# Optimization experiments

Measured on AMD Instinct MI355X. Metric: run time of the kernel, lower is better.

Reference implementation:

```python
import math
import jax, jax.numpy as jnp
import numpy as np

B, NQ, NKV, D, H = 32, 512, 512, 1024, 8
DH = D // H              # 128
N_COLS = 512             # n + 1
D_COL = math.ceil(2 * math.log2(N_COLS))  # 18


def setup_inputs() -> dict:
    key = jax.random.key(0)
    ks = jax.random.split(key, 8)
    s = 0.02
    return {
        "x_q": jax.random.normal(ks[0], (B, NQ, D), jnp.float32),
        "x_kv": jax.random.normal(ks[1], (B, NKV, D), jnp.float32),
        # sym_weight=True => W_tail is W_head (shared)
        "W_head_w": jax.random.normal(ks[2], (D, D), jnp.float32) * s,
        "W_head_b": jnp.zeros((D,), jnp.float32),
        "W_v_w": jax.random.normal(ks[3], (D, D), jnp.float32) * s,
        "W_v_b": jnp.zeros((D,), jnp.float32),
        "W_out_w": jax.random.normal(ks[4], (D, D), jnp.float32) * s,
        "W_out_b": jnp.zeros((D,), jnp.float32),
        "rel_emb": jnp.ones((H, DH), jnp.float32),
        "col_head": jax.random.normal(ks[5], (H, N_COLS, D_COL), jnp.float32) * 0.2,
        "col_tail": jax.random.normal(ks[6], (H, N_COLS, D_COL), jnp.float32) * 0.2,
    }


def _heads(x, W, b, h, dh):
    # Linear then split heads: [B, n, d] -> [B, H, n, dh]
    B_, n, _ = x.shape
    y = x @ W.T + b
    return y.reshape(B_, n, h, dh).transpose(0, 2, 1, 3)


def reference(x_q, x_kv, W_head_w, W_head_b, W_v_w, W_v_b,
              W_out_w, W_out_b, rel_emb, col_head, col_tail):
    Bb, nq, d = x_q.shape
    nkv = x_kv.shape[1]
    h, dh = rel_emb.shape

    f_head = _heads(x_q, W_head_w, W_head_b, h, dh) * rel_emb[None, :, None, :]
    f_tail = _heads(x_kv, W_head_w, W_head_b, h, dh) * rel_emb[None, :, None, :]  # W_tail = W_head (sym_weight)
    f_v = _heads(x_kv, W_v_w, W_v_b, h, dh)

    # content score: [B, H, nq, nkv]
    weight_score = jnp.einsum('bhqd,bhkd->bhqk', f_head, f_tail) / math.sqrt(dh)

    # learned column topology: [H, n_cols, n_cols]
    adj_logits = jnp.einsum('hqc,hkc->hqk', col_head, col_tail)
    eye = jnp.eye(adj_logits.shape[-1], dtype=bool)  # nsi: zero diagonal before softmax
    adj_logits = jnp.where(eye[None], 0.0, adj_logits)
    adj = jax.nn.softmax(adj_logits, axis=-1)[:, :nq, :nkv]

    adj_mask = (1.0 - adj) * -10000.0
    fr_graph = jax.nn.softmax(weight_score + adj_mask[None], axis=-1)

    x = jnp.einsum('bhqk,bhkd->bhqd', fr_graph, f_v)
    x = x.transpose(0, 2, 1, 3).reshape(Bb, nq, h * dh)
    x = x @ W_out_w.T + W_out_b
    return (x, fr_graph.reshape(Bb * h, nq, nkv))
```

## Files before the change

### kernel.cpp

```cpp
#include <hip/hip_runtime.h>

typedef __attribute__((ext_vector_type(8))) __bf16 bf8;
typedef __attribute__((ext_vector_type(4))) __bf16 bf4;
typedef __attribute__((ext_vector_type(4))) float f32x4;

#define DEVI static __device__ __forceinline__

DEVI void gload_lds16(const void* g, void* l) {
  __builtin_amdgcn_global_load_lds(
      (const __attribute__((address_space(1))) unsigned int*)g,
      (__attribute__((address_space(3))) unsigned int*)l, 16, 0, 0);
}

__global__ __launch_bounds__(256) void cvt_kernel(const float* __restrict__ in,
                                                  __bf16* __restrict__ out, int n4) {
  int stride = gridDim.x * blockDim.x;
  for (int i = blockIdx.x * blockDim.x + threadIdx.x; i < n4; i += stride) {
    f32x4 v = reinterpret_cast<const f32x4*>(in)[i];
    bf4 o;
    o[0] = (__bf16)v[0]; o[1] = (__bf16)v[1]; o[2] = (__bf16)v[2]; o[3] = (__bf16)v[3];
    reinterpret_cast<bf4*>(out)[i] = o;
  }
}

template <int MODE>
__global__ __launch_bounds__(256) void gemm_proj(
    const __bf16* __restrict__ A, const __bf16* __restrict__ Bw,
    const float* __restrict__ bias, const float* __restrict__ rel,
    __bf16* __restrict__ obf, float* __restrict__ of32) {
  __shared__ alignas(16) __bf16 As[128 * 64];
  __shared__ alignas(16) __bf16 Bs[128 * 64];
  const int tid = threadIdx.x;
  const int lane = tid & 63;
  const int wave = tid >> 6;
  const int wr = wave >> 1, wc = wave & 1;
  const int lr = lane & 15, lk = (lane >> 4) * 8;
  const int bm = blockIdx.x, bn = blockIdx.y;

  f32x4 acc[4][4];
#pragma unroll
  for (int i = 0; i < 4; ++i)
#pragma unroll
    for (int j = 0; j < 4; ++j)
#pragma unroll
      for (int e = 0; e < 4; ++e) acc[i][j][e] = 0.f;

  const __bf16* Ab = A + (size_t)bm * 128 * 1024;
  const __bf16* Bb = Bw + (size_t)bn * 128 * 1024;
  const int sr = tid >> 3;
  const int sc = (tid & 7) * 8;

  for (int kt = 0; kt < 1024; kt += 64) {
#pragma unroll
    for (int i = 0; i < 4; ++i) {
      gload_lds16(Ab + (size_t)(sr + i * 32) * 1024 + kt + sc, As + tid * 8 + i * 2048);
      gload_lds16(Bb + (size_t)(sr + i * 32) * 1024 + kt + sc, Bs + tid * 8 + i * 2048);
    }
    __syncthreads();
#pragma unroll
    for (int kk = 0; kk < 64; kk += 32) {
      bf8 a[4], b[4];
#pragma unroll
      for (int mi = 0; mi < 4; ++mi)
        a[mi] = *reinterpret_cast<const bf8*>(&As[(wr * 64 + mi * 16 + lr) * 64 + kk + lk]);
#pragma unroll
      for (int ni = 0; ni < 4; ++ni)
        b[ni] = *reinterpret_cast<const bf8*>(&Bs[(wc * 64 + ni * 16 + lr) * 64 + kk + lk]);
#pragma unroll
      for (int mi = 0; mi < 4; ++mi)
#pragma unroll
        for (int ni = 0; ni < 4; ++ni)
          acc[mi][ni] = __builtin_amdgcn_mfma_f32_16x16x32_bf16(a[mi], b[ni], acc[mi][ni], 0, 0, 0);
    }
    __syncthreads();
  }

  const int mBase = bm * 128 + wr * 64;
  const int nBase = bn * 128 + wc * 64;
#pragma unroll
  for (int mi = 0; mi < 4; ++mi) {
#pragma unroll
    for (int ni = 0; ni < 4; ++ni) {
      const int n = nBase + ni * 16 + lr;
#pragma unroll
      for (int r = 0; r < 4; ++r) {
        const int m = mBase + mi * 16 + (lane >> 4) * 4 + r;
        float v = acc[mi][ni][r] + bias[n];
        if (MODE == 0) v *= rel[n];
        if (MODE == 2) {
          of32[(size_t)m * 1024 + n] = v;
        } else if (MODE == 0) {
          size_t idx = ((size_t)((m >> 9) * 8 + (n >> 7))) * 65536 +
                       (size_t)(m & 511) * 128 + (n & 127);
          obf[idx] = (__bf16)v;
        } else {
          size_t idx = ((size_t)((m >> 9) * 8 + (n >> 7))) * 65536 +
                       (size_t)(n & 127) * 512 + (m & 511);
          obf[idx] = (__bf16)v;
        }
      }
    }
  }
}

__global__ __launch_bounds__(256) void adj_kernel(const float* __restrict__ ch_all,
                                                  const float* __restrict__ ct_all,
                                                  float* __restrict__ adjT) {
  const int wave = threadIdx.x >> 6, lane = threadIdx.x & 63;
  const int row = blockIdx.x * 4 + wave;
  const int h = row >> 9, i = row & 511;
  float ch[18];
  const float* chp = ch_all + ((size_t)h * 512 + i) * 18;
#pragma unroll
  for (int t = 0; t < 18; ++t) ch[t] = chp[t];
  float e[8];
  float m = -1e30f;
#pragma unroll
  for (int jj = 0; jj < 8; ++jj) {
    const int j = jj * 64 + lane;
    const float* ctp = ct_all + ((size_t)h * 512 + j) * 18;
    float d = 0.f;
#pragma unroll
    for (int t = 0; t < 18; ++t) d += ch[t] * ctp[t];
    if (j == i) d = 0.f;
    e[jj] = d;
    m = fmaxf(m, d);
  }
#pragma unroll
  for (int off = 32; off >= 1; off >>= 1) m = fmaxf(m, __shfl_xor(m, off));
  float s = 0.f;
#pragma unroll
  for (int jj = 0; jj < 8; ++jj) { e[jj] = __expf(e[jj] - m); s += e[jj]; }
#pragma unroll
  for (int off = 32; off >= 1; off >>= 1) s += __shfl_xor(s, off);
  const float inv = 10000.f / s;
  float* op = adjT + (size_t)h * 262144 + i;
#pragma unroll
  for (int jj = 0; jj < 8; ++jj) op[(size_t)(jj * 64 + lane) * 512] = e[jj] * inv;
}

__global__ __launch_bounds__(256, 3) void fused_attn_kernel(
    const __bf16* __restrict__ fh, const __bf16* __restrict__ ft,
    const __bf16* __restrict__ fvT, const float* __restrict__ adjT,
    float* __restrict__ fr, __bf16* __restrict__ ctx) {
  __shared__ alignas(16) __bf16 Bt[128 * 128];
  __shared__ alignas(16) __bf16 Pl[4][16 * 128];
  const int tid = threadIdx.x;
  const int l = tid & 63, w = tid >> 6;
  const int bh = blockIdx.x;
  const int qt = blockIdx.y;
  const int b = bh >> 3, h = bh & 7;
  const int wrow = qt * 64 + w * 16;
  const int lr = l & 15;
  const int khi = l >> 4;

  const int srow = tid >> 4;
  const int scc = (tid & 15) ^ (srow & 7);

  bf8 afr[4];
  {
    const __bf16* ap = fh + (size_t)bh * 65536 + (size_t)(wrow + lr) * 128 + khi * 8;
#pragma unroll
    for (int kk4 = 0; kk4 < 4; ++kk4)
      afr[kk4] = *reinterpret_cast<const bf8*>(ap + kk4 * 32);
  }

  f32x4 acc[32];
#pragma unroll
  for (int n = 0; n < 32; ++n)
#pragma unroll
    for (int e = 0; e < 4; ++e) acc[n][e] = 0.f;

  const __bf16* ftb = ft + (size_t)bh * 65536;
#pragma unroll
  for (int kt = 0; kt < 4; ++kt) {
#pragma unroll
    for (int i = 0; i < 8; ++i)
      gload_lds16(ftb + (size_t)(kt * 128 + i * 16 + srow) * 128 + scc * 8,
                  Bt + i * 2048 + tid * 8);
    __syncthreads();
#pragma unroll
    for (int kk4 = 0; kk4 < 4; ++kk4) {
      bf8 bfr[8];
#pragma unroll
      for (int n2 = 0; n2 < 8; ++n2)
        bfr[n2] = *reinterpret_cast<const bf8*>(
            &Bt[(n2 * 16 + lr) * 128 + ((kk4 * 4 + khi) ^ (lr & 7)) * 8]);
#pragma unroll
      for (int n2 = 0; n2 < 8; ++n2)
        acc[kt * 8 + n2] =
            __builtin_amdgcn_mfma_f32_16x16x32_bf16(afr[kk4], bfr[n2], acc[kt * 8 + n2], 0, 0, 0);
    }
    __syncthreads();
  }

  const float scale = 0.08838834764831845f;
  const float* adjTp = adjT + (size_t)h * 262144;
  float mrow[4] = {-1e30f, -1e30f, -1e30f, -1e30f};
#pragma unroll
  for (int n = 0; n < 32; ++n) {
    const int col = n * 16 + lr;
    f32x4 av = *reinterpret_cast<const f32x4*>(adjTp + (size_t)col * 512 + wrow + khi * 4);
#pragma unroll
    for (int r = 0; r < 4; ++r) {
      float v = acc[n][r] * scale + av[r];
      acc[n][r] = v;
      mrow[r] = fmaxf(mrow[r], v);
    }
  }
#pragma unroll
  for (int r = 0; r < 4; ++r)
#pragma unroll
    for (int off = 1; off <= 8; off <<= 1) mrow[r] = fmaxf(mrow[r], __shfl_xor(mrow[r], off));
  float srw[4] = {0.f, 0.f, 0.f, 0.f};
#pragma unroll
  for (int n = 0; n < 32; ++n)
#pragma unroll
    for (int r = 0; r < 4; ++r) {
      float e = __expf(acc[n][r] - mrow[r]);
      acc[n][r] = e;
      srw[r] += e;
    }
#pragma unroll
  for (int r = 0; r < 4; ++r)
#pragma unroll
    for (int off = 1; off <= 8; off <<= 1) srw[r] += __shfl_xor(srw[r], off);
  float inv[4];
#pragma unroll
  for (int r = 0; r < 4; ++r) inv[r] = 1.f / srw[r];
#pragma unroll
  for (int n = 0; n < 32; ++n)
#pragma unroll
    for (int r = 0; r < 4; ++r) acc[n][r] *= inv[r];

  const __bf16* fvb = fvT + (size_t)bh * 65536;
#pragma unroll
  for (int i = 0; i < 8; ++i)
    gload_lds16(fvb + (size_t)(i * 16 + srow) * 512 + scc * 8, Bt + i * 2048 + tid * 8);

  {
    float* frb = fr + (size_t)bh * 262144;
#pragma unroll
    for (int n = 0; n < 32; ++n) {
      const int col = n * 16 + lr;
#pragma unroll
      for (int r = 0; r < 4; ++r)
        frb[(size_t)(wrow + khi * 4 + r) * 512 + col] = acc[n][r];
    }
  }

  f32x4 acc2[8];
#pragma unroll
  for (int n2 = 0; n2 < 8; ++n2)
#pragma unroll
    for (int e = 0; e < 4; ++e) acc2[n2][e] = 0.f;

  __bf16* Pw = &Pl[w][0];
#pragma unroll
  for (int kt = 0; kt < 4; ++kt) {
#pragma unroll
    for (int n2 = 0; n2 < 8; ++n2) {
      const int colc = n2 * 2 + (lr >> 3);
      const int cl = lr & 7;
#pragma unroll
      for (int r = 0; r < 4; ++r) {
        const int q = khi * 4 + r;
        Pw[q * 128 + ((colc ^ (q & 7)) * 8) + cl] = (__bf16)acc[kt * 8 + n2][r];
      }
    }
    __syncthreads();
#pragma unroll
    for (int kk4 = 0; kk4 < 4; ++kk4) {
      bf8 pa = *reinterpret_cast<const bf8*>(
          &Pw[lr * 128 + ((kk4 * 4 + khi) ^ (lr & 7)) * 8]);
      bf8 bfr[8];
#pragma unroll
      for (int n2 = 0; n2 < 8; ++n2)
        bfr[n2] = *reinterpret_cast<const bf8*>(
            &Bt[(n2 * 16 + lr) * 128 + ((kk4 * 4 + khi) ^ (lr & 7)) * 8]);
#pragma unroll
      for (int n2 = 0; n2 < 8; ++n2)
        acc2[n2] = __builtin_amdgcn_mfma_f32_16x16x32_bf16(pa, bfr[n2], acc2[n2], 0, 0, 0);
    }
    __syncthreads();
    if (kt < 3) {
      const int ktn = kt + 1;
#pragma unroll
      for (int i = 0; i < 8; ++i)
        gload_lds16(fvb + (size_t)(i * 16 + srow) * 512 + ktn * 128 + scc * 8,
                    Bt + i * 2048 + tid * 8);
    }
  }

#pragma unroll
  for (int n2 = 0; n2 < 8; ++n2) {
    const int c = n2 * 16 + lr;
#pragma unroll
    for (int r = 0; r < 4; ++r) {
      const int q = wrow + khi * 4 + r;
      ctx[(size_t)(b * 512 + q) * 1024 + h * 128 + c] = (__bf16)acc2[n2][r];
    }
  }
}

extern "C" void kernel_launch(void* const* d_in, const int* in_sizes, int n_in,
                              void* d_out, int out_size, void* d_ws, size_t ws_size,
                              hipStream_t stream) {
  const float* x_q  = (const float*)d_in[0];
  const float* x_kv = (const float*)d_in[1];
  const float* Wh   = (const float*)d_in[2];
  const float* bh   = (const float*)d_in[3];
  const float* Wv   = (const float*)d_in[4];
  const float* bv   = (const float*)d_in[5];
  const float* Wo   = (const float*)d_in[6];
  const float* bo   = (const float*)d_in[7];
  const float* rel  = (const float*)d_in[8];
  const float* colh = (const float*)d_in[9];
  const float* colt = (const float*)d_in[10];

  float* out = (float*)d_out;
  float* fr  = out + 16777216;

  __bf16* xq_bf  = (__bf16*)d_ws;
  __bf16* xkv_bf = xq_bf + 16777216;
  __bf16* Wh_bf  = xkv_bf + 16777216;
  __bf16* Wv_bf  = Wh_bf + 1048576;
  __bf16* Wo_bf  = Wv_bf + 1048576;
  __bf16* fhead  = Wo_bf + 1048576;
  __bf16* ftail  = fhead + 16777216;
  __bf16* fvT    = ftail + 16777216;
  float*  adjT   = (float*)(fvT + 16777216);
  __bf16* ctx    = (__bf16*)(adjT + 2097152);

  cvt_kernel<<<4096, 256, 0, stream>>>(x_q, xq_bf, 4194304);
  cvt_kernel<<<4096, 256, 0, stream>>>(x_kv, xkv_bf, 4194304);
  cvt_kernel<<<1024, 256, 0, stream>>>(Wh, Wh_bf, 262144);
  cvt_kernel<<<1024, 256, 0, stream>>>(Wv, Wv_bf, 262144);
  cvt_kernel<<<1024, 256, 0, stream>>>(Wo, Wo_bf, 262144);

  dim3 gp(128, 8);
  gemm_proj<0><<<gp, 256, 0, stream>>>(xq_bf, Wh_bf, bh, rel, fhead, nullptr);
  gemm_proj<0><<<gp, 256, 0, stream>>>(xkv_bf, Wh_bf, bh, rel, ftail, nullptr);
  gemm_proj<1><<<gp, 256, 0, stream>>>(xkv_bf, Wv_bf, bv, nullptr, fvT, nullptr);

  adj_kernel<<<1024, 256, 0, stream>>>(colh, colt, adjT);

  fused_attn_kernel<<<dim3(256, 8), 256, 0, stream>>>(fhead, ftail, fvT, adjT, fr, ctx);

  gemm_proj<2><<<gp, 256, 0, stream>>>(ctx, Wo_bf, bo, nullptr, nullptr, out);
}
```

Baseline: 895.5 us.

## Store adjacency mask in bf16, remap attention grid, add MFMA priority hints

The adjacency mask bias is now stored as bf16 with a constant offset subtracted, so values stay near zero and keep bf16 precision. This halves the mask read traffic in the attention kernel. The attention grid is remapped so blocks of the same head sit together, which should improve L2 reuse of the per-head mask. s_setprio hints are placed around the MFMA loops. The constant shift leaves the softmax unchanged, but bf16 rounding adds some error to the mask.

```diff
diff --git a/kernel.cpp b/kernel.cpp
--- a/kernel.cpp
+++ b/kernel.cpp
@@ -105,7 +105,7 @@
 
 __global__ __launch_bounds__(256) void adj_kernel(const float* __restrict__ ch_all,
                                                   const float* __restrict__ ct_all,
-                                                  float* __restrict__ adjT) {
+                                                  __bf16* __restrict__ adjT) {
   const int wave = threadIdx.x >> 6, lane = threadIdx.x & 63;
   const int row = blockIdx.x * 4 + wave;
   const int h = row >> 9, i = row & 511;
@@ -134,22 +134,24 @@
 #pragma unroll
   for (int off = 32; off >= 1; off >>= 1) s += __shfl_xor(s, off);
   const float inv = 10000.f / s;
-  float* op = adjT + (size_t)h * 262144 + i;
-#pragma unroll
-  for (int jj = 0; jj < 8; ++jj) op[(size_t)(jj * 64 + lane) * 512] = e[jj] * inv;
+  __bf16* op = adjT + (size_t)h * 262144 + i;
+#pragma unroll
+  for (int jj = 0; jj < 8; ++jj)
+    op[(size_t)(jj * 64 + lane) * 512] = (__bf16)(e[jj] * inv - 19.53125f);
 }
 
 __global__ __launch_bounds__(256, 3) void fused_attn_kernel(
     const __bf16* __restrict__ fh, const __bf16* __restrict__ ft,
-    const __bf16* __restrict__ fvT, const float* __restrict__ adjT,
+    const __bf16* __restrict__ fvT, const __bf16* __restrict__ adjT,
     float* __restrict__ fr, __bf16* __restrict__ ctx) {
   __shared__ alignas(16) __bf16 Bt[128 * 128];
   __shared__ alignas(16) __bf16 Pl[4][16 * 128];
   const int tid = threadIdx.x;
   const int l = tid & 63, w = tid >> 6;
-  const int bh = blockIdx.x;
-  const int qt = blockIdx.y;
-  const int b = bh >> 3, h = bh & 7;
+  const int b = blockIdx.x;
+  const int h = blockIdx.y >> 3;
+  const int qt = blockIdx.y & 7;
+  const int bh = b * 8 + h;
   const int wrow = qt * 64 + w * 16;
   const int lr = l & 15;
   const int khi = l >> 4;
@@ -179,6 +181,7 @@
       gload_lds16(ftb + (size_t)(kt * 128 + i * 16 + srow) * 128 + scc * 8,
                   Bt + i * 2048 + tid * 8);
     __syncthreads();
+    __builtin_amdgcn_s_setprio(1);
 #pragma unroll
     for (int kk4 = 0; kk4 < 4; ++kk4) {
       bf8 bfr[8];
@@ -191,19 +194,20 @@
         acc[kt * 8 + n2] =
             __builtin_amdgcn_mfma_f32_16x16x32_bf16(afr[kk4], bfr[n2], acc[kt * 8 + n2], 0, 0, 0);
     }
+    __builtin_amdgcn_s_setprio(0);
     __syncthreads();
   }
 
   const float scale = 0.08838834764831845f;
-  const float* adjTp = adjT + (size_t)h * 262144;
+  const __bf16* adjTp = adjT + (size_t)h * 262144;
   float mrow[4] = {-1e30f, -1e30f, -1e30f, -1e30f};
 #pragma unroll
   for (int n = 0; n < 32; ++n) {
     const int col = n * 16 + lr;
-    f32x4 av = *reinterpret_cast<const f32x4*>(adjTp + (size_t)col * 512 + wrow + khi * 4);
+    bf4 av4 = *reinterpret_cast<const bf4*>(adjTp + (size_t)col * 512 + wrow + khi * 4);
 #pragma unroll
     for (int r = 0; r < 4; ++r) {
-      float v = acc[n][r] * scale + av[r];
+      float v = acc[n][r] * scale + (float)av4[r];
       acc[n][r] = v;
       mrow[r] = fmaxf(mrow[r], v);
     }
@@ -269,6 +273,7 @@
       }
     }
     __syncthreads();
+    __builtin_amdgcn_s_setprio(1);
 #pragma unroll
     for (int kk4 = 0; kk4 < 4; ++kk4) {
       bf8 pa = *reinterpret_cast<const bf8*>(
@@ -282,6 +287,7 @@
       for (int n2 = 0; n2 < 8; ++n2)
         acc2[n2] = __builtin_amdgcn_mfma_f32_16x16x32_bf16(pa, bfr[n2], acc2[n2], 0, 0, 0);
     }
+    __builtin_amdgcn_s_setprio(0);
     __syncthreads();
     if (kt < 3) {
       const int ktn = kt + 1;
@@ -329,8 +335,8 @@
   __bf16* fhead  = Wo_bf + 1048576;
   __bf16* ftail  = fhead + 16777216;
   __bf16* fvT    = ftail + 16777216;
-  float*  adjT   = (float*)(fvT + 16777216);
-  __bf16* ctx    = (__bf16*)(adjT + 2097152);
+  __bf16* adjT   = fvT + 16777216;
+  __bf16* ctx    = adjT + 2097152;
 
   cvt_kernel<<<4096, 256, 0, stream>>>(x_q, xq_bf, 4194304);
   cvt_kernel<<<4096, 256, 0, stream>>>(x_kv, xkv_bf, 4194304);
@@ -345,7 +351,7 @@
 
   adj_kernel<<<1024, 256, 0, stream>>>(colh, colt, adjT);
 
-  fused_attn_kernel<<<dim3(256, 8), 256, 0, stream>>>(fhead, ftail, fvT, adjT, fr, ctx);
+  fused_attn_kernel<<<dim3(32, 64), 256, 0, stream>>>(fhead, ftail, fvT, adjT, fr, ctx);
 
   gemm_proj<2><<<gp, 256, 0, stream>>>(ctx, Wo_bf, bo, nullptr, nullptr, out);
 }
```

After: 878.1 us. Within noise of the previous version (-1.9%).
